# Optimization experiments

Measured on AMD Instinct MI355X. Metric: run time of the kernel, lower is better.

The kernel has to match this reference:

```python
import jax, jax.numpy as jnp
import numpy as np

NUM_NODES = 20000
NUM_RELATIONS = 32
HIDDEN = 128
EMB = 16
NUM_EDGES = 600000


def setup_inputs() -> dict:
    key = jax.random.key(0)
    ks = jax.random.split(key, 8)
    edge_index = jax.random.randint(ks[0], (2, NUM_EDGES), 0, NUM_NODES, dtype=jnp.int64)
    edge_type = jax.random.randint(ks[1], (NUM_EDGES,), 0, NUM_RELATIONS, dtype=jnp.int64)
    node_emb = jax.random.normal(ks[2], (NUM_NODES, EMB), dtype=jnp.float32)
    W1 = jax.random.normal(ks[3], (NUM_RELATIONS, EMB, HIDDEN), dtype=jnp.float32) * (1.0 / np.sqrt(EMB))
    root1 = jax.random.normal(ks[4], (EMB, HIDDEN), dtype=jnp.float32) * (1.0 / np.sqrt(EMB))
    b1 = jnp.zeros((HIDDEN,), dtype=jnp.float32)
    W2 = jax.random.normal(ks[5], (NUM_RELATIONS, HIDDEN, HIDDEN), dtype=jnp.float32) * (1.0 / np.sqrt(HIDDEN))
    root2 = jax.random.normal(ks[6], (HIDDEN, HIDDEN), dtype=jnp.float32) * (1.0 / np.sqrt(HIDDEN))
    b2 = jnp.zeros((HIDDEN,), dtype=jnp.float32)
    return {"edge_index": edge_index, "edge_type": edge_type, "node_emb": node_emb,
            "W1": W1, "root1": root1, "b1": b1, "W2": W2, "root2": root2, "b2": b2}


def rgcn_layer(x, edge_index, edge_type, W, root, bias):
    # PyG RGCNConv: per-relation transform, per-(dst, relation) MEAN aggregation,
    # summed over relations, plus root transform and bias.
    src, dst = edge_index[0], edge_index[1]
    # mean normalization per (dst, relation) segment
    seg = dst * NUM_RELATIONS + edge_type                      # [E]
    counts = jax.ops.segment_sum(jnp.ones(seg.shape, jnp.float32), seg,
                                 num_segments=NUM_NODES * NUM_RELATIONS)
    inv = jnp.where(counts > 0, 1.0 / counts, 0.0)
    # transform every node by every relation weight: [N, R, H]
    xr = jnp.einsum('nf,rfh->nrh', x, W)
    msg = xr[src, edge_type] * inv[seg][:, None]               # [E, H]
    agg = jax.ops.segment_sum(msg, dst, num_segments=NUM_NODES)  # [N, H]
    return agg + x @ root + bias


def reference(edge_index, edge_type, node_emb, W1, root1, b1, W2, root2, b2):
    h = rgcn_layer(node_emb, edge_index, edge_type, W1, root1, b1)
    h = jax.nn.relu(h)
    h = rgcn_layer(h, edge_index, edge_type, W2, root2, b2)
    return h
```

## Files before the change

### kernel.cpp

```cpp
#include <hip/hip_runtime.h>
#include <hip/hip_bf16.h>

#define N_NODES 20000
#define N_REL 32
#define HID 128
#define EMB 16
#define N_EDGES 600000
#define NB (N_NODES * N_REL)

typedef __attribute__((ext_vector_type(8))) short  bf8v;
typedef __attribute__((ext_vector_type(8))) unsigned short us8v;
typedef __attribute__((ext_vector_type(4))) unsigned short us4v;
typedef __attribute__((ext_vector_type(4))) float  f4v;

__device__ __forceinline__ unsigned short f2b(float f) {
    __hip_bfloat16 h = __float2bfloat16(f);
    return __builtin_bit_cast(unsigned short, h);
}
__device__ __forceinline__ float b2f(unsigned short u) {
    unsigned int x = ((unsigned int)u) << 16;
    return __builtin_bit_cast(float, x);
}

__device__ __forceinline__ void lds_barrier() {
    asm volatile("s_waitcnt lgkmcnt(0)\n\ts_barrier" ::: "memory");
}

#define R_W2 (N_REL * HID * HID)
#define R_XB (N_NODES * EMB)
#define R_W1 (N_REL * EMB * HID)
#define R_R1 (HID * 32)
#define R_R2 (HID * HID)
#define R_HIST N_EDGES
#define PRE_TOT (R_W2 + R_XB + R_W1 + R_R1 + R_R2 + R_HIST)

__global__ __launch_bounds__(256) void pre1_k(
    const int* __restrict__ dst, const int* __restrict__ et,
    const float* __restrict__ x, const float* __restrict__ W1,
    const float* __restrict__ root1, const float* __restrict__ W2,
    const float* __restrict__ root2,
    int* __restrict__ hist,
    unsigned short* __restrict__ xb, unsigned short* __restrict__ w1t,
    unsigned short* __restrict__ r1t, unsigned short* __restrict__ w2t,
    unsigned short* __restrict__ r2t) {
    int i = blockIdx.x * 256 + threadIdx.x;
    if (i < R_W2) {
        int r = i >> 14, k = (i >> 7) & 127, n = i & 127;
        int kb = r * 4 + (k >> 5), q = (k >> 3) & 3, j = k & 7;
        int ct8 = n >> 4, m16 = n & 15;
        w2t[(size_t)kb * 4096 + ct8 * 512 + m16 * 32 + q * 8 + j] = f2b(W2[i]);
        return;
    }
    i -= R_W2;
    if (i < R_XB) { xb[i] = f2b(x[i]); return; }
    i -= R_XB;
    if (i < R_W1) {
        int rel = i >> 11, kk = (i >> 7) & 15, n = i & 127;
        int kb = rel >> 1, k = ((rel & 1) << 4) + kk;
        int q = k >> 3, j = k & 7, ct8 = n >> 4, m16 = n & 15;
        w1t[kb * 4096 + ct8 * 512 + m16 * 32 + q * 8 + j] = f2b(W1[i]);
        return;
    }
    i -= R_W1;
    if (i < R_R1) {
        int k = i >> 7, n = i & 127;
        int q = k >> 3, j = k & 7, ct8 = n >> 4, m16 = n & 15;
        r1t[ct8 * 512 + m16 * 32 + q * 8 + j] =
            (k < EMB) ? f2b(root1[k * 128 + n]) : (unsigned short)0;
        return;
    }
    i -= R_R1;
    if (i < R_R2) {
        int k = i >> 7, n = i & 127;
        int ks = k >> 5, q = (k >> 3) & 3, j = k & 7, ct8 = n >> 4, m16 = n & 15;
        r2t[(ks * 8 + ct8) * 512 + m16 * 32 + q * 8 + j] = f2b(root2[i]);
        return;
    }
    i -= R_R2;
    if (i < R_HIST) atomicAdd(&hist[dst[i] * N_REL + et[i]], 1);
}

__global__ void scan1_k(const int* __restrict__ hist, int* __restrict__ binoff,
                        int* __restrict__ bsum, float* __restrict__ inv) {
    __shared__ int sh[256];
    const int t = threadIdx.x;
    const int base = blockIdx.x * 1024 + t * 4;
    int4 h4 = *(const int4*)(hist + base);
    float4 iv4;
    iv4.x = h4.x > 0 ? 1.0f / h4.x : 0.0f;
    iv4.y = h4.y > 0 ? 1.0f / h4.y : 0.0f;
    iv4.z = h4.z > 0 ? 1.0f / h4.z : 0.0f;
    iv4.w = h4.w > 0 ? 1.0f / h4.w : 0.0f;
    *(float4*)(inv + base) = iv4;
    int ts = h4.x + h4.y + h4.z + h4.w;
    sh[t] = ts;
    __syncthreads();
    for (int o = 1; o < 256; o <<= 1) {
        int v = (t >= o) ? sh[t - o] : 0;
        __syncthreads();
        sh[t] += v;
        __syncthreads();
    }
    int exc = sh[t] - ts;
    binoff[base + 0] = exc;
    binoff[base + 1] = exc + h4.x;
    binoff[base + 2] = exc + h4.x + h4.y;
    binoff[base + 3] = exc + h4.x + h4.y + h4.z;
    if (t == 255) bsum[blockIdx.x] = sh[255];
}

__global__ void scan2_k(const int* __restrict__ bsum, int* __restrict__ bbase) {
    __shared__ int sh[1024];
    const int t = threadIdx.x;
    int v = (t < 625) ? bsum[t] : 0;
    sh[t] = v;
    __syncthreads();
    for (int o = 1; o < 1024; o <<= 1) {
        int u = (t >= o) ? sh[t - o] : 0;
        __syncthreads();
        sh[t] += u;
        __syncthreads();
    }
    if (t < 625) bbase[t] = sh[t] - v;
}

__global__ void scan3_k(int* __restrict__ binoff, const int* __restrict__ bbase,
                        int* __restrict__ cursors) {
    int i = blockIdx.x * 256 + threadIdx.x;
    if (i < NB) {
        int v = binoff[i] + bbase[i >> 10];
        binoff[i] = v;
        cursors[i] = v;
    }
    if (i == 0) binoff[NB] = N_EDGES;
}

__global__ void scatter_k(const int* __restrict__ src, const int* __restrict__ dst,
                          const int* __restrict__ et, int* __restrict__ cursors,
                          int* __restrict__ ssrc) {
    int e = blockIdx.x * 256 + threadIdx.x;
    if (e < 4) ssrc[N_EDGES + e] = 0;
    if (e < N_EDGES) {
        int b = dst[e] * N_REL + et[e];
        int p = atomicAdd(&cursors[b], 1);
        ssrc[p] = src[e];
    }
}

template<int ROWG, int NRC, int NIT, int KR, int OUT>
__global__ __launch_bounds__(256) void gemm_f(
    const int* __restrict__ binoff, const float* __restrict__ inv,
    const int* __restrict__ ssrc,
    const unsigned short* __restrict__ G,
    const unsigned short* __restrict__ Bw,
    const unsigned short* __restrict__ Br,
    float* __restrict__ outf, unsigned short* __restrict__ fout,
    const float* __restrict__ bias) {

    constexpr int RG  = NRC * NIT;
    constexpr int KT  = (NRC * ROWG) / 32;
    constexpr int NCH = 256 / (32 * NRC);
    constexpr int CW  = ROWG / NCH;
    constexpr int CP8 = CW / 8;
    constexpr int LSS = NRC * ROWG + 8;
    static_assert(NCH * CW == ROWG, "chunk covering must be exact");
    static_assert(CP8 * 8 == CW, "16B unit covering");
    static_assert(KT * 32 == NRC * ROWG, "K must be a multiple of 32");
    static_assert(32 * NRC * NCH == 256, "all threads gather");
    static_assert(RG == 32, "single group covers all relations");

    __shared__ __align__(16) unsigned short As[2][32 * LSS];
    __shared__ int   smO[32 * (RG + 1)];
    __shared__ float smI[32 * RG];

    const int t = threadIdx.x;
    const int w = t >> 6, lane = t & 63;
    const int q = lane >> 4, m16 = lane & 15;
    const int d0 = blockIdx.x * 32;
    const int colb = w * 32;
    const int cb16 = colb >> 4;
    const int fo = m16 * 32 + q * 8;
    const int brow = t / (NRC * NCH);
    const int rsub = (t / NCH) % NRC;
    const int gcc  = t % NCH;
    const int mb  = brow * (RG + 1) + rsub;
    const int mbI = brow * RG + rsub;
    int uo[CP8];
#pragma unroll
    for (int j = 0; j < CP8; ++j) uo[j] = (gcc + j * NCH) * 8;
    const int lbase = brow * LSS + rsub * ROWG;

    for (int i = t; i < 32 * (RG + 1); i += 256) {
        int row = i / (RG + 1), rr = i % (RG + 1);
        smO[i] = binoff[(d0 + row) * N_REL + rr];
    }
    for (int i = t; i < 32 * RG; i += 256) {
        int row = i / RG, rr = i % RG;
        smI[i] = inv[(d0 + row) * N_REL + rr];
    }
    lds_barrier();

    f4v acc[2][2];
#pragma unroll
    for (int rt = 0; rt < 2; ++rt)
#pragma unroll
        for (int ct = 0; ct < 2; ++ct) acc[rt][ct] = f4v{0.f, 0.f, 0.f, 0.f};

    us8v gE[4][CP8];
#pragma unroll
    for (int e = 0; e < 4; ++e)
#pragma unroll
        for (int j = 0; j < CP8; ++j) gE[e][j] = us8v{};
    int sx[4] = {0, 0, 0, 0};

    {
        const int so = smO[mb], cnt = smO[mb + 1] - so;
        int s0 = ssrc[so], s1 = ssrc[so + 1], s2 = ssrc[so + 2], s3 = ssrc[so + 3];
        if (cnt >= 1) {
            const unsigned short* gp = G + (size_t)s0 * ROWG;
#pragma unroll
            for (int j = 0; j < CP8; ++j) gE[0][j] = *(const us8v*)(gp + uo[j]);
        }
        if (cnt >= 2) {
            const unsigned short* gp = G + (size_t)s1 * ROWG;
#pragma unroll
            for (int j = 0; j < CP8; ++j) gE[1][j] = *(const us8v*)(gp + uo[j]);
        }
        if (cnt >= 3) {
            const unsigned short* gp = G + (size_t)s2 * ROWG;
#pragma unroll
            for (int j = 0; j < CP8; ++j) gE[2][j] = *(const us8v*)(gp + uo[j]);
        }
        if (cnt >= 4) {
            const unsigned short* gp = G + (size_t)s3 * ROWG;
#pragma unroll
            for (int j = 0; j < CP8; ++j) gE[3][j] = *(const us8v*)(gp + uo[j]);
        }
        if (NIT > 1) {
            const int so1 = smO[mb + NRC];
            sx[0] = ssrc[so1]; sx[1] = ssrc[so1 + 1];
            sx[2] = ssrc[so1 + 2]; sx[3] = ssrc[so1 + 3];
        }
    }

    bf8v bfr[2][KT];
    {
#pragma unroll
        for (int ct = 0; ct < 2; ++ct) {
#pragma unroll
            for (int ks = 0; ks < KT; ++ks)
                bfr[ct][ks] = *(const bf8v*)(Bw + ((size_t)ks * 8 + cb16 + ct) * 512 + fo);
        }
    }

#pragma unroll 2
    for (int it = 0; it < NIT; ++it) {
        unsigned short* Ab = As[it & 1];
        {
            const int so = smO[mb + it * NRC], eo = smO[mb + it * NRC + 1];
            const int cnt = eo - so;
            const float m2 = cnt >= 2 ? 1.f : 0.f;
            const float m3 = cnt >= 3 ? 1.f : 0.f;
            const float m4 = cnt >= 4 ? 1.f : 0.f;
            float a[CW];
#pragma unroll
            for (int j = 0; j < CP8; ++j)
#pragma unroll
                for (int k = 0; k < 8; ++k)
                    a[j * 8 + k] = b2f(gE[0][j][k]) + m2 * b2f(gE[1][j][k])
                                 + m3 * b2f(gE[2][j][k]) + m4 * b2f(gE[3][j][k]);
            for (int p = so + 4; p < eo; ++p) {
                const unsigned short* gp = G + (size_t)ssrc[p] * ROWG;
#pragma unroll
                for (int j = 0; j < CP8; ++j) {
                    us8v g = *(const us8v*)(gp + uo[j]);
#pragma unroll
                    for (int k = 0; k < 8; ++k) a[j * 8 + k] += b2f(g[k]);
                }
            }
            const float iv = smI[mbI + it * NRC];
            unsigned short* wp = &Ab[lbase];
#pragma unroll
            for (int j = 0; j < CP8; ++j) {
                us8v sv;
#pragma unroll
                for (int k = 0; k < 8; ++k) sv[k] = f2b(a[j * 8 + k] * iv);
                *(us8v*)(wp + uo[j]) = sv;
            }

            if (it + 1 < NIT) {
                const int b1o = mb + (it + 1) * NRC;
                const int c1 = smO[b1o + 1] - smO[b1o];
                if (c1 >= 1) {
                    const unsigned short* gp = G + (size_t)sx[0] * ROWG;
#pragma unroll
                    for (int j = 0; j < CP8; ++j) gE[0][j] = *(const us8v*)(gp + uo[j]);
                }
                if (c1 >= 2) {
                    const unsigned short* gp = G + (size_t)sx[1] * ROWG;
#pragma unroll
                    for (int j = 0; j < CP8; ++j) gE[1][j] = *(const us8v*)(gp + uo[j]);
                }
                if (c1 >= 3) {
                    const unsigned short* gp = G + (size_t)sx[2] * ROWG;
#pragma unroll
                    for (int j = 0; j < CP8; ++j) gE[2][j] = *(const us8v*)(gp + uo[j]);
                }
                if (c1 >= 4) {
                    const unsigned short* gp = G + (size_t)sx[3] * ROWG;
#pragma unroll
                    for (int j = 0; j < CP8; ++j) gE[3][j] = *(const us8v*)(gp + uo[j]);
                }
                if (it + 2 < NIT) {
                    const int so2 = smO[mb + (it + 2) * NRC];
                    sx[0] = ssrc[so2]; sx[1] = ssrc[so2 + 1];
                    sx[2] = ssrc[so2 + 2]; sx[3] = ssrc[so2 + 3];
                }
            }
        }
        lds_barrier();

#pragma unroll
        for (int rt = 0; rt < 2; ++rt) {
            const unsigned short* ar = &Ab[(m16 + 16 * rt) * LSS];
#pragma unroll
            for (int ks = 0; ks < KT; ++ks) {
                bf8v af = *(const bf8v*)(ar + ks * 32 + q * 8);
                acc[rt][0] = __builtin_amdgcn_mfma_f32_16x16x32_bf16(af, bfr[0][ks], acc[rt][0], 0, 0, 0);
                acc[rt][1] = __builtin_amdgcn_mfma_f32_16x16x32_bf16(af, bfr[1][ks], acc[rt][1], 0, 0, 0);
            }
        }

        if (it + 1 < NIT) {
            const int kb0 = ((it + 1) * NRC * ROWG) >> 5;
#pragma unroll
            for (int ct = 0; ct < 2; ++ct) {
#pragma unroll
                for (int ks = 0; ks < KT; ++ks)
                    bfr[ct][ks] = *(const bf8v*)(Bw + ((size_t)(kb0 + ks) * 8 + cb16 + ct) * 512 + fo);
            }
        } else {
#pragma unroll
            for (int ct = 0; ct < 2; ++ct) {
#pragma unroll
                for (int ks = 0; ks < KR; ++ks)
                    bfr[ct][ks] = *(const bf8v*)(Br + ((size_t)ks * 8 + cb16 + ct) * 512 + fo);
            }
        }
    }

    {
#pragma unroll
        for (int rt = 0; rt < 2; ++rt) {
            const unsigned short* gr = G + (size_t)(d0 + m16 + 16 * rt) * ROWG;
#pragma unroll
            for (int ks = 0; ks < KR; ++ks) {
                bf8v af;
                if constexpr (ROWG % 32 == 0) {
                    af = *(const bf8v*)(gr + ks * 32 + q * 8);
                } else {
                    af = bf8v{0, 0, 0, 0, 0, 0, 0, 0};
                    if (ks * 32 + q * 8 + 8 <= ROWG)
                        af = *(const bf8v*)(gr + ks * 32 + q * 8);
                }
                acc[rt][0] = __builtin_amdgcn_mfma_f32_16x16x32_bf16(af, bfr[0][ks], acc[rt][0], 0, 0, 0);
                acc[rt][1] = __builtin_amdgcn_mfma_f32_16x16x32_bf16(af, bfr[1][ks], acc[rt][1], 0, 0, 0);
            }
        }
    }

    if constexpr (OUT == 1) {
#pragma unroll
        for (int ct = 0; ct < 2; ++ct) {
            const int col = colb + 16 * ct + m16;
            const float bb = bias[col];
#pragma unroll
            for (int rt = 0; rt < 2; ++rt) {
#pragma unroll
                for (int g = 0; g < 4; ++g) {
                    const int rr = 16 * rt + q * 4 + g;
                    fout[(size_t)(d0 + rr) * HID + col] =
                        f2b(fmaxf(acc[rt][ct][g] + bb, 0.0f));
                }
            }
        }
    } else {
#pragma unroll
        for (int ct = 0; ct < 2; ++ct) {
            const int col = colb + 16 * ct + m16;
            const float bb = bias[col];
#pragma unroll
            for (int rt = 0; rt < 2; ++rt) {
#pragma unroll
                for (int g = 0; g < 4; ++g) {
                    const int rr = 16 * rt + q * 4 + g;
                    outf[(size_t)(d0 + rr) * HID + col] = acc[rt][ct][g] + bb;
                }
            }
        }
    }
}

extern "C" void kernel_launch(void* const* d_in, const int* in_sizes, int n_in,
                              void* d_out, int out_size, void* d_ws, size_t ws_size,
                              hipStream_t stream) {
    const int*   ei    = (const int*)d_in[0];
    const int*   et    = (const int*)d_in[1];
    const float* x     = (const float*)d_in[2];
    const float* W1    = (const float*)d_in[3];
    const float* root1 = (const float*)d_in[4];
    const float* b1    = (const float*)d_in[5];
    const float* W2    = (const float*)d_in[6];
    const float* root2 = (const float*)d_in[7];
    const float* b2    = (const float*)d_in[8];
    float* out = (float*)d_out;

    char* ws = (char*)d_ws;
    size_t off = 0;
    auto alloc = [&](size_t bytes) { void* p = ws + off; off = (off + bytes + 63) & ~(size_t)63; return p; };
    int*   hist    = (int*)  alloc((size_t)NB * 4);
    int*   binoff  = (int*)  alloc((size_t)(NB + 1) * 4);
    int*   cursors = (int*)  alloc((size_t)NB * 4);
    float* inv     = (float*)alloc((size_t)NB * 4);
    int*   bsum    = (int*)  alloc(625 * 4);
    int*   bbase   = (int*)  alloc(625 * 4);
    int*   ssrc    = (int*)  alloc((size_t)(N_EDGES + 4) * 4);
    unsigned short* xb  = (unsigned short*)alloc((size_t)N_NODES * EMB * 2);
    unsigned short* h1b = (unsigned short*)alloc((size_t)N_NODES * HID * 2);
    unsigned short* w1t = (unsigned short*)alloc((size_t)R_W1 * 2);
    unsigned short* r1t = (unsigned short*)alloc((size_t)HID * 32 * 2);
    unsigned short* w2t = (unsigned short*)alloc((size_t)N_REL * HID * HID * 2);
    unsigned short* r2t = (unsigned short*)alloc((size_t)HID * HID * 2);

    const int* src = ei;
    const int* dst = ei + N_EDGES;

    hipMemsetAsync(hist, 0, (size_t)NB * 4, stream);
    pre1_k<<<(PRE_TOT + 255) / 256, 256, 0, stream>>>(
        dst, et, x, W1, root1, W2, root2, hist, xb, w1t, r1t, w2t, r2t);
    scan1_k<<<NB / 1024, 256, 0, stream>>>(hist, binoff, bsum, inv);
    scan2_k<<<1, 1024, 0, stream>>>(bsum, bbase);
    scan3_k<<<(NB + 255) / 256, 256, 0, stream>>>(binoff, bbase, cursors);
    scatter_k<<<(N_EDGES + 255) / 256, 256, 0, stream>>>(src, dst, et, cursors, ssrc);

    gemm_f<16, 8, 4, 1, 1><<<dim3(625, 1), 256, 0, stream>>>(
        binoff, inv, ssrc, xb, w1t, r1t, nullptr, h1b, b1);

    gemm_f<128, 1, 32, 4, 2><<<dim3(625, 1), 256, 0, stream>>>(
        binoff, inv, ssrc, h1b, w2t, r2t, out, nullptr, b2);
}
```

Measured before the change: 232.2 us.

## Drop scan fixup kernel and halve rows per GEMM block

Removes the third scan pass. scan1 now writes local bin offsets to both binoff and cursors, and the per-1024-block base is added lazily in scatter and in the GEMM offset loads. The GEMM kernels are templated on rows per block and launched with 16 rows across 1250 blocks instead of 32 rows across 625, so more blocks are available to fill the CUs. The cost is an extra bbase lookup per offset load and less reuse of the B fragments per block.

```diff
diff --git a/kernel.cpp b/kernel.cpp
--- a/kernel.cpp
+++ b/kernel.cpp
@@ -10,7 +10,6 @@
 
 typedef __attribute__((ext_vector_type(8))) short  bf8v;
 typedef __attribute__((ext_vector_type(8))) unsigned short us8v;
-typedef __attribute__((ext_vector_type(4))) unsigned short us4v;
 typedef __attribute__((ext_vector_type(4))) float  f4v;
 
 __device__ __forceinline__ unsigned short f2b(float f) {
@@ -81,6 +80,7 @@
 }
 
 __global__ void scan1_k(const int* __restrict__ hist, int* __restrict__ binoff,
+                        int* __restrict__ cursors,
                         int* __restrict__ bsum, float* __restrict__ inv) {
     __shared__ int sh[256];
     const int t = threadIdx.x;
@@ -102,14 +102,18 @@
         __syncthreads();
     }
     int exc = sh[t] - ts;
-    binoff[base + 0] = exc;
-    binoff[base + 1] = exc + h4.x;
-    binoff[base + 2] = exc + h4.x + h4.y;
-    binoff[base + 3] = exc + h4.x + h4.y + h4.z;
+    int4 b4;
+    b4.x = exc;
+    b4.y = exc + h4.x;
+    b4.z = exc + h4.x + h4.y;
+    b4.w = exc + h4.x + h4.y + h4.z;
+    *(int4*)(binoff + base) = b4;
+    *(int4*)(cursors + base) = b4;
     if (t == 255) bsum[blockIdx.x] = sh[255];
 }
 
-__global__ void scan2_k(const int* __restrict__ bsum, int* __restrict__ bbase) {
+__global__ void scan2_k(const int* __restrict__ bsum, int* __restrict__ bbase,
+                        int* __restrict__ binoff) {
     __shared__ int sh[1024];
     const int t = threadIdx.x;
     int v = (t < 625) ? bsum[t] : 0;
@@ -122,35 +126,26 @@
         __syncthreads();
     }
     if (t < 625) bbase[t] = sh[t] - v;
-}
-
-__global__ void scan3_k(int* __restrict__ binoff, const int* __restrict__ bbase,
-                        int* __restrict__ cursors) {
-    int i = blockIdx.x * 256 + threadIdx.x;
-    if (i < NB) {
-        int v = binoff[i] + bbase[i >> 10];
-        binoff[i] = v;
-        cursors[i] = v;
-    }
-    if (i == 0) binoff[NB] = N_EDGES;
+    if (t == 625) bbase[625] = N_EDGES;
+    if (t == 626) binoff[NB] = 0;
 }
 
 __global__ void scatter_k(const int* __restrict__ src, const int* __restrict__ dst,
                           const int* __restrict__ et, int* __restrict__ cursors,
-                          int* __restrict__ ssrc) {
+                          const int* __restrict__ bbase, int* __restrict__ ssrc) {
     int e = blockIdx.x * 256 + threadIdx.x;
     if (e < 4) ssrc[N_EDGES + e] = 0;
     if (e < N_EDGES) {
         int b = dst[e] * N_REL + et[e];
-        int p = atomicAdd(&cursors[b], 1);
+        int p = atomicAdd(&cursors[b], 1) + bbase[b >> 10];
         ssrc[p] = src[e];
     }
 }
 
-template<int ROWG, int NRC, int NIT, int KR, int OUT>
+template<int ROWS, int ROWG, int NRC, int NIT, int KR, int OUT>
 __global__ __launch_bounds__(256) void gemm_f(
-    const int* __restrict__ binoff, const float* __restrict__ inv,
-    const int* __restrict__ ssrc,
+    const int* __restrict__ binoff, const int* __restrict__ bbase,
+    const float* __restrict__ inv, const int* __restrict__ ssrc,
     const unsigned short* __restrict__ G,
     const unsigned short* __restrict__ Bw,
     const unsigned short* __restrict__ Br,
@@ -159,24 +154,26 @@
 
     constexpr int RG  = NRC * NIT;
     constexpr int KT  = (NRC * ROWG) / 32;
-    constexpr int NCH = 256 / (32 * NRC);
+    constexpr int NCH = 256 / (ROWS * NRC);
     constexpr int CW  = ROWG / NCH;
     constexpr int CP8 = CW / 8;
     constexpr int LSS = NRC * ROWG + 8;
+    constexpr int RT  = ROWS / 16;
     static_assert(NCH * CW == ROWG, "chunk covering must be exact");
     static_assert(CP8 * 8 == CW, "16B unit covering");
     static_assert(KT * 32 == NRC * ROWG, "K must be a multiple of 32");
-    static_assert(32 * NRC * NCH == 256, "all threads gather");
+    static_assert(ROWS * NRC * NCH == 256, "all threads gather");
     static_assert(RG == 32, "single group covers all relations");
-
-    __shared__ __align__(16) unsigned short As[2][32 * LSS];
-    __shared__ int   smO[32 * (RG + 1)];
-    __shared__ float smI[32 * RG];
+    static_assert(RT * 16 == ROWS, "rows multiple of 16");
+
+    __shared__ __align__(16) unsigned short As[2][ROWS * LSS];
+    __shared__ int   smO[ROWS * (RG + 1)];
+    __shared__ float smI[ROWS * RG];
 
     const int t = threadIdx.x;
     const int w = t >> 6, lane = t & 63;
     const int q = lane >> 4, m16 = lane & 15;
-    const int d0 = blockIdx.x * 32;
+    const int d0 = blockIdx.x * ROWS;
     const int colb = w * 32;
     const int cb16 = colb >> 4;
     const int fo = m16 * 32 + q * 8;
@@ -190,19 +187,20 @@
     for (int j = 0; j < CP8; ++j) uo[j] = (gcc + j * NCH) * 8;
     const int lbase = brow * LSS + rsub * ROWG;
 
-    for (int i = t; i < 32 * (RG + 1); i += 256) {
+    for (int i = t; i < ROWS * (RG + 1); i += 256) {
         int row = i / (RG + 1), rr = i % (RG + 1);
-        smO[i] = binoff[(d0 + row) * N_REL + rr];
-    }
-    for (int i = t; i < 32 * RG; i += 256) {
+        int bi = (d0 + row) * N_REL + rr;
+        smO[i] = binoff[bi] + bbase[bi >> 10];
+    }
+    for (int i = t; i < ROWS * RG; i += 256) {
         int row = i / RG, rr = i % RG;
         smI[i] = inv[(d0 + row) * N_REL + rr];
     }
     lds_barrier();
 
-    f4v acc[2][2];
-#pragma unroll
-    for (int rt = 0; rt < 2; ++rt)
+    f4v acc[RT][2];
+#pragma unroll
+    for (int rt = 0; rt < RT; ++rt)
 #pragma unroll
         for (int ct = 0; ct < 2; ++ct) acc[rt][ct] = f4v{0.f, 0.f, 0.f, 0.f};
 
@@ -321,7 +319,7 @@
         lds_barrier();
 
 #pragma unroll
-        for (int rt = 0; rt < 2; ++rt) {
+        for (int rt = 0; rt < RT; ++rt) {
             const unsigned short* ar = &Ab[(m16 + 16 * rt) * LSS];
 #pragma unroll
             for (int ks = 0; ks < KT; ++ks) {
@@ -351,7 +349,7 @@
 
     {
 #pragma unroll
-        for (int rt = 0; rt < 2; ++rt) {
+        for (int rt = 0; rt < RT; ++rt) {
             const unsigned short* gr = G + (size_t)(d0 + m16 + 16 * rt) * ROWG;
 #pragma unroll
             for (int ks = 0; ks < KR; ++ks) {
@@ -375,7 +373,7 @@
             const int col = colb + 16 * ct + m16;
             const float bb = bias[col];
 #pragma unroll
-            for (int rt = 0; rt < 2; ++rt) {
+            for (int rt = 0; rt < RT; ++rt) {
 #pragma unroll
                 for (int g = 0; g < 4; ++g) {
                     const int rr = 16 * rt + q * 4 + g;
@@ -390,7 +388,7 @@
             const int col = colb + 16 * ct + m16;
             const float bb = bias[col];
 #pragma unroll
-            for (int rt = 0; rt < 2; ++rt) {
+            for (int rt = 0; rt < RT; ++rt) {
 #pragma unroll
                 for (int g = 0; g < 4; ++g) {
                     const int rr = 16 * rt + q * 4 + g;
@@ -423,7 +421,7 @@
     int*   cursors = (int*)  alloc((size_t)NB * 4);
     float* inv     = (float*)alloc((size_t)NB * 4);
     int*   bsum    = (int*)  alloc(625 * 4);
-    int*   bbase   = (int*)  alloc(625 * 4);
+    int*   bbase   = (int*)  alloc(626 * 4);
     int*   ssrc    = (int*)  alloc((size_t)(N_EDGES + 4) * 4);
     unsigned short* xb  = (unsigned short*)alloc((size_t)N_NODES * EMB * 2);
     unsigned short* h1b = (unsigned short*)alloc((size_t)N_NODES * HID * 2);
@@ -438,14 +436,13 @@
     hipMemsetAsync(hist, 0, (size_t)NB * 4, stream);
     pre1_k<<<(PRE_TOT + 255) / 256, 256, 0, stream>>>(
         dst, et, x, W1, root1, W2, root2, hist, xb, w1t, r1t, w2t, r2t);
-    scan1_k<<<NB / 1024, 256, 0, stream>>>(hist, binoff, bsum, inv);
-    scan2_k<<<1, 1024, 0, stream>>>(bsum, bbase);
-    scan3_k<<<(NB + 255) / 256, 256, 0, stream>>>(binoff, bbase, cursors);
-    scatter_k<<<(N_EDGES + 255) / 256, 256, 0, stream>>>(src, dst, et, cursors, ssrc);
-
-    gemm_f<16, 8, 4, 1, 1><<<dim3(625, 1), 256, 0, stream>>>(
-        binoff, inv, ssrc, xb, w1t, r1t, nullptr, h1b, b1);
-
-    gemm_f<128, 1, 32, 4, 2><<<dim3(625, 1), 256, 0, stream>>>(
-        binoff, inv, ssrc, h1b, w2t, r2t, out, nullptr, b2);
-}
+    scan1_k<<<NB / 1024, 256, 0, stream>>>(hist, binoff, cursors, bsum, inv);
+    scan2_k<<<1, 1024, 0, stream>>>(bsum, bbase, binoff);
+    scatter_k<<<(N_EDGES + 255) / 256, 256, 0, stream>>>(src, dst, et, cursors, bbase, ssrc);
+
+    gemm_f<16, 16, 8, 4, 1, 1><<<dim3(1250, 1), 256, 0, stream>>>(
+        binoff, bbase, inv, ssrc, xb, w1t, r1t, nullptr, h1b, b1);
+
+    gemm_f<16, 128, 1, 32, 4, 2><<<dim3(1250, 1), 256, 0, stream>>>(
+        binoff, bbase, inv, ssrc, h1b, w2t, r2t, out, nullptr, b2);
+}
```

Result: slower. 266.6 us (+14.8%).
